# Kernel tuning notes

Hardware: AMD Instinct MI355X
Metric: run time of the kernel (lower is better)

Reference implementation:

```python
import jax, jax.numpy as jnp
import numpy as np

N_NODES = 100000
D = 128


def _sage_layer(h, src, dst, w_self, w_neigh, b):
    # GraphSAGE mean aggregation: mean of neighbor (src) features per dst node.
    msg = h[src]                                            # [E, D] gather
    agg = jax.ops.segment_sum(msg, dst, num_segments=N_NODES)  # [N, D]
    deg = jax.ops.segment_sum(jnp.ones(src.shape, h.dtype), dst, num_segments=N_NODES)
    mean = agg / jnp.maximum(deg, 1.0)[:, None]
    return h @ w_self + mean @ w_neigh + b


def setup_inputs() -> dict:
    key = jax.random.key(0)
    ks = jax.random.split(key, 16)
    E = 1600000
    inp = {
        "feat": jax.random.normal(ks[0], (N_NODES, D), jnp.float32),
        "edge0_src": jax.random.randint(ks[1], (E,), 0, N_NODES),
        "edge0_dst": jax.random.randint(ks[2], (E,), 0, N_NODES),
        "edge1_src": jax.random.randint(ks[3], (E,), 0, N_NODES),
        "edge1_dst": jax.random.randint(ks[4], (E,), 0, N_NODES),
        "pos_src": jax.random.randint(ks[5], (100000,), 0, N_NODES),
        "pos_dst": jax.random.randint(ks[6], (100000,), 0, N_NODES),
        "neg_src": jax.random.randint(ks[7], (500000,), 0, N_NODES),
        "neg_dst": jax.random.randint(ks[8], (500000,), 0, N_NODES),
        # learned parameters
        "w_proj": jax.random.normal(ks[9], (D, D), jnp.float32) / np.sqrt(D),
        "b_proj": jnp.zeros((D,), jnp.float32),
        "w_self1": jax.random.normal(ks[10], (D, D), jnp.float32) / np.sqrt(D),
        "w_neigh1": jax.random.normal(ks[11], (D, D), jnp.float32) / np.sqrt(D),
        "b1": jnp.zeros((D,), jnp.float32),
        "w_self2": jax.random.normal(ks[12], (D, D), jnp.float32) / np.sqrt(D),
        "w_neigh2": jax.random.normal(ks[13], (D, D), jnp.float32) / np.sqrt(D),
        "b2": jnp.zeros((D,), jnp.float32),
    }
    return inp


def reference(feat, edge0_src, edge0_dst, edge1_src, edge1_dst,
              pos_src, pos_dst, neg_src, neg_dst,
              w_proj, b_proj, w_self1, w_neigh1, b1, w_self2, w_neigh2, b2):
    # ProjectionLayer: per-node linear + ReLU on blocks[0].srcdata['feature']
    h = jax.nn.relu(feat @ w_proj + b_proj)
    # GNNLayer: one SAGE-mean layer per block
    h = jax.nn.relu(_sage_layer(h, edge0_src, edge0_dst, w_self1, w_neigh1, b1))
    h = _sage_layer(h, edge1_src, edge1_dst, w_self2, w_neigh2, b2)
    # PredictionLayer: dot-product edge scoring on pos_graph / neg_graph
    pos_score = jnp.sum(h[pos_src] * h[pos_dst], axis=-1)
    neg_score = jnp.sum(h[neg_src] * h[neg_dst], axis=-1)
    return (pos_score, neg_score)
```

## Files before the change

kernel.cpp:

```cpp
#include <hip/hip_runtime.h>
#include <hip/hip_bf16.h>

#define NN 100000
#define DD 128

#define NPB 512
#define NB 196
#define CAPB 12288
#define PA_BLOCKS 196

typedef unsigned short ushort_t;
typedef unsigned int uint_t;
typedef __attribute__((ext_vector_type(8))) short bf16x8;
typedef __attribute__((ext_vector_type(4))) float f32x4;

__device__ __forceinline__ ushort_t f2bf(float f) {
    uint_t u = __builtin_bit_cast(uint_t, f);
    u += 0x7FFFu + ((u >> 16) & 1u);
    return (ushort_t)(u >> 16);
}
__device__ __forceinline__ uint_t pack2bf(float a, float b) {
    return (uint_t)f2bf(a) | ((uint_t)f2bf(b) << 16);
}
__device__ __forceinline__ float bflo(uint_t v) {
    return __builtin_bit_cast(float, v << 16);
}
__device__ __forceinline__ float bfhi(uint_t v) {
    return __builtin_bit_cast(float, v & 0xFFFF0000u);
}

__device__ __forceinline__ void gload16(const ushort_t* g, ushort_t* l) {
    __builtin_amdgcn_global_load_lds(
        (const __attribute__((address_space(1))) void*)g,
        (__attribute__((address_space(3))) void*)l,
        16, 0, 0);
}

#define PREP_W_BLOCKS 320
#define PREP_Z_BLOCKS 3
__global__ __launch_bounds__(256) void prep(
    const float* __restrict__ w_proj,
    const float* __restrict__ w_self1, const float* __restrict__ w_neigh1,
    const float* __restrict__ w_self2, const float* __restrict__ w_neigh2,
    ushort_t* __restrict__ wtp, ushort_t* __restrict__ wt1,
    ushort_t* __restrict__ wt2, int* __restrict__ bcnt,
    ushort_t* __restrict__ h1pad, ushort_t* __restrict__ h2pad)
{
    const int bid = blockIdx.x;
    const int tid = threadIdx.x;
    if (bid < PREP_W_BLOCKS) {
        int which = bid >> 6;
        int t = (bid & 63) * 256 + tid;
        int n = t >> 7, k = t & 127;
        float v;
        ushort_t* d;
        switch (which) {
            case 0: v = w_proj  [(size_t)k * 128 + n]; d = wtp + (size_t)n * 128 + k;       break;
            case 1: v = w_self1 [(size_t)k * 128 + n]; d = wt1 + (size_t)n * 256 + k;       break;
            case 2: v = w_neigh1[(size_t)k * 128 + n]; d = wt1 + (size_t)n * 256 + 128 + k; break;
            case 3: v = w_self2 [(size_t)k * 128 + n]; d = wt2 + (size_t)n * 256 + k;       break;
            default:v = w_neigh2[(size_t)k * 128 + n]; d = wt2 + (size_t)n * 256 + 128 + k; break;
        }
        *d = f2bf(v);
    } else if (bid < PREP_W_BLOCKS + 2) {
        int i = (bid - PREP_W_BLOCKS) * 256 + tid;
        if (i < 2 * NB) bcnt[i] = 0;
    } else {
        uint_t* p1 = (uint_t*)h1pad;
        uint_t* p2 = (uint_t*)h2pad;
        if (tid < 64) p1[tid] = 0;
        else if (tid < 128) p2[tid - 64] = 0;
    }
}

template <bool RELU, bool TWO, bool CVT>
__global__ __launch_bounds__(256, 4) void gemm_bf16(
    const void* __restrict__ Av, const ushort_t* __restrict__ Bm,
    const ushort_t* __restrict__ W, const float* __restrict__ bias,
    ushort_t* __restrict__ outp)
{
    __shared__ char smem[32768];
    ushort_t* Ot = (ushort_t*)smem;

    const int tid  = threadIdx.x;
    const int lane = tid & 63;
    const int wav  = tid >> 6;
    const int row0 = blockIdx.x * 128;
    const int m0   = (wav & 1) * 64;
    const int n0   = (wav >> 1) * 64;
    const int KTOT = TWO ? 256 : 128;
    const int NCH  = TWO ? 8 : 4;

    f32x4 acc[4][4];
#pragma unroll
    for (int i = 0; i < 4; ++i)
#pragma unroll
        for (int j = 0; j < 4; ++j) acc[i][j] = (f32x4){0.f, 0.f, 0.f, 0.f};

    const int cl = lane & 15;
    const int q  = lane >> 4;

    if constexpr (CVT) {
        ushort_t* At = (ushort_t*)smem;
        ushort_t* Wt = (ushort_t*)(smem + 8192);
#pragma unroll 1
        for (int ch = 0; ch < NCH; ++ch) {
            const int kA = (ch & 3) * 32;
            const int kW = ch * 32;

            if (ch) __syncthreads();
#pragma unroll
            for (int j = 0; j < 2; ++j) {
                int cb = (j * 4 + wav) * 64;
                int c  = cb + lane;
                int r  = c >> 2, k2 = c & 3;
                gload16(W + (size_t)r * KTOT + kW + k2 * 8, Wt + cb * 8);
            }
            uint4 av[2];
            const float* fp = (const float*)Av;
#pragma unroll
            for (int j = 0; j < 2; ++j) {
                int g = tid + 256 * j;
                int r = g >> 2;
                int c = (g & 3) * 8;
                int grow = row0 + r;
                if (grow >= NN) grow = NN - 1;
                float4 f0 = *(const float4*)(fp + (size_t)grow * DD + kA + c);
                float4 f1 = *(const float4*)(fp + (size_t)grow * DD + kA + c + 4);
                av[j].x = pack2bf(f0.x, f0.y);
                av[j].y = pack2bf(f0.z, f0.w);
                av[j].z = pack2bf(f1.x, f1.y);
                av[j].w = pack2bf(f1.z, f1.w);
            }
#pragma unroll
            for (int j = 0; j < 2; ++j) {
                int g = tid + 256 * j;
                int r = g >> 2;
                int c = (g & 3) * 8;
                *(uint4*)(&At[r * 32 + c]) = av[j];
            }
            __syncthreads();

            bf16x8 af[4], bfr[4];
#pragma unroll
            for (int i = 0; i < 4; ++i)
                af[i] = *(const bf16x8*)(&At[(m0 + i * 16 + cl) * 32 + q * 8]);
#pragma unroll
            for (int j = 0; j < 4; ++j)
                bfr[j] = *(const bf16x8*)(&Wt[(n0 + j * 16 + cl) * 32 + q * 8]);
#pragma unroll
            for (int i = 0; i < 4; ++i)
#pragma unroll
                for (int j = 0; j < 4; ++j)
                    acc[i][j] = __builtin_amdgcn_mfma_f32_16x16x32_bf16(
                        af[i], bfr[j], acc[i][j], 0, 0, 0);
        }
    } else {
        auto STAGE = [&](int ch, int buf) {
            const bool second = TWO && (ch >= 4);
            const int kA = (ch & 3) * 32;
            const int kW = ch * 32;
            ushort_t* At = (ushort_t*)(smem + buf * 16384);
            ushort_t* Wt = At + 4096;
            const ushort_t* sp = second ? Bm : (const ushort_t*)Av;
#pragma unroll
            for (int j = 0; j < 2; ++j) {
                int cb = (j * 4 + wav) * 64;
                int c  = cb + lane;
                int r  = c >> 2, k2 = c & 3;
                int grow = row0 + r;
                if (grow >= NN) grow = NN - 1;
                gload16(sp + (size_t)grow * DD + kA + k2 * 8, At + cb * 8);
                gload16(W + (size_t)r * KTOT + kW + k2 * 8, Wt + cb * 8);
            }
        };
        auto COMPUTE = [&](int buf) {
            ushort_t* At = (ushort_t*)(smem + buf * 16384);
            ushort_t* Wt = At + 4096;
            bf16x8 af[4], bfr[4];
#pragma unroll
            for (int i = 0; i < 4; ++i)
                af[i] = *(const bf16x8*)(&At[(m0 + i * 16 + cl) * 32 + q * 8]);
#pragma unroll
            for (int j = 0; j < 4; ++j)
                bfr[j] = *(const bf16x8*)(&Wt[(n0 + j * 16 + cl) * 32 + q * 8]);
#pragma unroll
            for (int i = 0; i < 4; ++i)
#pragma unroll
                for (int j = 0; j < 4; ++j)
                    acc[i][j] = __builtin_amdgcn_mfma_f32_16x16x32_bf16(
                        af[i], bfr[j], acc[i][j], 0, 0, 0);
        };

        STAGE(0, 0);
        asm volatile("s_waitcnt vmcnt(0)" ::: "memory");
        __builtin_amdgcn_s_barrier();
        int cur = 0;
#pragma unroll 1
        for (int ch = 0; ch < NCH - 1; ++ch) {
            STAGE(ch + 1, cur ^ 1);
            COMPUTE(cur);
            asm volatile("s_waitcnt vmcnt(0)" ::: "memory");
            __builtin_amdgcn_s_barrier();
            cur ^= 1;
        }
        COMPUTE(cur);
    }

    __syncthreads();
#pragma unroll
    for (int j = 0; j < 4; ++j) {
        int c = n0 + j * 16 + cl;
        float bv = bias[c];
#pragma unroll
        for (int i = 0; i < 4; ++i) {
#pragma unroll
            for (int reg = 0; reg < 4; ++reg) {
                int r = m0 + i * 16 + 4 * q + reg;
                float v = acc[i][j][reg] + bv;
                if constexpr (RELU) v = fmaxf(v, 0.f);
                Ot[r * 128 + c] = f2bf(v);
            }
        }
    }
    __syncthreads();
    int rows = NN - row0; if (rows > 128) rows = 128;
    for (int t = tid; t < rows * 16; t += 256) {
        int r = t >> 4, c8 = (t & 15) * 8;
        *(uint4*)(outp + (size_t)(row0 + r) * DD + c8) =
            *(const uint4*)(&Ot[r * 128 + c8]);
    }
}

__global__ __launch_bounds__(256) void partA2(
    const int* __restrict__ e0s, const int* __restrict__ e0d, int E0,
    const int* __restrict__ e1s, const int* __restrict__ e1d, int E1,
    int* __restrict__ bcnt, uint_t* __restrict__ pairs)
{
    __shared__ int hist[NB];
    __shared__ int base[NB];
    const int tid  = threadIdx.x;
    const int half = blockIdx.x >= PA_BLOCKS;
    const int* __restrict__ src = half ? e1s : e0s;
    const int* __restrict__ dst = half ? e1d : e0d;
    const int E = half ? E1 : E0;
    int* bc = bcnt + half * NB;
    uint_t* pp = pairs + (size_t)half * NB * CAPB;
    const int blk = blockIdx.x - half * PA_BLOCKS;
    const int chunk = (E + PA_BLOCKS - 1) / PA_BLOCKS;
    const int ea = blk * chunk;
    int eb = ea + chunk; if (eb > E) eb = E;

    for (int b = tid; b < NB; b += 256) hist[b] = 0;
    __syncthreads();
    for (int e = ea + tid; e < eb; e += 256)
        atomicAdd(&hist[dst[e] >> 9], 1);
    __syncthreads();
    for (int b = tid; b < NB; b += 256) {
        base[b] = atomicAdd(&bc[b], hist[b]);
        hist[b] = 0;
    }
    __syncthreads();
    for (int e = ea + tid; e < eb; e += 256) {
        int d = dst[e];
        int b = d >> 9;
        int off = atomicAdd(&hist[b], 1);
        int p = base[b] + off;
        if (p < CAPB)
            pp[(size_t)b * CAPB + p] =
                ((uint_t)(d & (NPB - 1)) << 17) | (uint_t)src[e];
    }
}

__global__ __launch_bounds__(256, 2) void partB(
    uint_t* __restrict__ pairs, const int* __restrict__ bcnt,
    int* __restrict__ counts, int* __restrict__ offs)
{
    __shared__ int cnt[NPB];
    __shared__ int loff[NPB];
    __shared__ int ssc[256];
    __shared__ int image[CAPB];

    const int tid  = threadIdx.x;
    const int half = blockIdx.x >= NB;
    const int b    = blockIdx.x - half * NB;
    const int n0   = b << 9;
    int nb = NN - n0; if (nb > NPB) nb = NPB;
    int tot = bcnt[half * NB + b]; if (tot > CAPB) tot = CAPB;
    uint_t* pb = pairs + (size_t)(half * NB + b) * CAPB;
    const int gbase = (half * NB + b) * CAPB;
    int* cnts  = counts + (size_t)half * NN;
    int* offsl = offs   + (size_t)half * NN;

    for (int n = tid; n < NPB; n += 256) cnt[n] = 0;
    __syncthreads();
    for (int i = tid; i < tot; i += 256)
        atomicAdd(&cnt[pb[i] >> 17], 1);
    __syncthreads();

    int a0 = cnt[2 * tid], a1 = cnt[2 * tid + 1];
    int s = a0 + a1;
    ssc[tid] = s;
    __syncthreads();
    for (int off = 1; off < 256; off <<= 1) {
        int t = 0;
        if (tid >= off) t = ssc[tid - off];
        __syncthreads();
        if (tid >= off) ssc[tid] += t;
        __syncthreads();
    }
    int pre = ssc[tid] - s;
    loff[2 * tid]     = pre;
    loff[2 * tid + 1] = pre + a0;
    __syncthreads();

    for (int n = tid; n < nb; n += 256) {
        cnts[n0 + n]  = cnt[n];
        offsl[n0 + n] = gbase + loff[n];
    }
    for (int n = tid; n < NPB; n += 256) cnt[n] = 0;
    __syncthreads();

    for (int i = tid; i < tot; i += 256) {
        uint_t p = pb[i];
        int ln  = p >> 17;
        int pos = loff[ln] + atomicAdd(&cnt[ln], 1);
        image[pos] = (int)(p & 0x1FFFFu);
    }
    __syncthreads();
    for (int i = tid; i < tot; i += 256) pb[i] = (uint_t)image[i];
}

#define AGG_ISSUE(V, J)                                                   \
    do {                                                                  \
        int s_[8];                                                        \
        _Pragma("unroll")                                                 \
        for (int u = 0; u < 8; ++u) {                                     \
            int jj = (J) + u;                                             \
            int jc = jj < cnt ? jj : cnt - 1;                             \
            int sv = (int)csr[start + jc];                                \
            s_[u] = jj < cnt ? sv : NN;                                   \
        }                                                                 \
        _Pragma("unroll")                                                 \
        for (int u = 0; u < 8; ++u)                                       \
            V[u] = *(const uint4*)(hl + (size_t)s_[u] * DD);              \
    } while (0)

#define AGG_ACCUM(V)                                                      \
    do {                                                                  \
        _Pragma("unroll")                                                 \
        for (int u = 0; u < 8; ++u) {                                     \
            a0 += bflo(V[u].x); a1 += bfhi(V[u].x);                       \
            a2 += bflo(V[u].y); a3 += bfhi(V[u].y);                       \
            a4 += bflo(V[u].z); a5 += bfhi(V[u].z);                       \
            a6 += bflo(V[u].w); a7 += bfhi(V[u].w);                       \
        }                                                                 \
    } while (0)

__global__ __launch_bounds__(256) void aggregate_bf16(
    const ushort_t* __restrict__ h, const uint_t* __restrict__ csr,
    const int* __restrict__ offs, const int* __restrict__ counts,
    ushort_t* __restrict__ mean, int nn)
{
    int gid  = blockIdx.x * 256 + threadIdx.x;
    int node = gid >> 4;
    if (node >= nn) return;
    int lane  = gid & 15;
    int start = offs[node];
    int cnt   = counts[node];
    const ushort_t* __restrict__ hl = h + lane * 8;

    float a0 = 0.f, a1 = 0.f, a2 = 0.f, a3 = 0.f;
    float a4 = 0.f, a5 = 0.f, a6 = 0.f, a7 = 0.f;

    int nbt = (cnt + 7) >> 3;
    if (nbt > 0) {
        uint4 va[8], vb[8];
        AGG_ISSUE(va, 0);
        int j = 8, b = 1;
        for (; b + 1 < nbt; b += 2) {
            AGG_ISSUE(vb, j); j += 8;
            AGG_ACCUM(va);
            AGG_ISSUE(va, j); j += 8;
            AGG_ACCUM(vb);
        }
        if (b < nbt) {
            AGG_ISSUE(vb, j);
            AGG_ACCUM(va);
            AGG_ACCUM(vb);
        } else {
            AGG_ACCUM(va);
        }
    }

    float rinv = 1.0f / (float)(cnt > 1 ? cnt : 1);
    uint4 o;
    o.x = pack2bf(a0 * rinv, a1 * rinv);
    o.y = pack2bf(a2 * rinv, a3 * rinv);
    o.z = pack2bf(a4 * rinv, a5 * rinv);
    o.w = pack2bf(a6 * rinv, a7 * rinv);
    *(uint4*)(mean + (size_t)node * DD + lane * 8) = o;
}

__device__ __forceinline__ float dot8(uint4 a, uint4 b) {
    return bflo(a.x) * bflo(b.x) + bfhi(a.x) * bfhi(b.x)
         + bflo(a.y) * bflo(b.y) + bfhi(a.y) * bfhi(b.y)
         + bflo(a.z) * bflo(b.z) + bfhi(a.z) * bfhi(b.z)
         + bflo(a.w) * bflo(b.w) + bfhi(a.w) * bfhi(b.w);
}

__global__ __launch_bounds__(256) void score_both(
    const ushort_t* __restrict__ h,
    const int* __restrict__ ps, const int* __restrict__ pd,
    const int* __restrict__ ns, const int* __restrict__ nd,
    float* __restrict__ out, int EP, int TE)
{
    int gid = blockIdx.x * 256 + threadIdx.x;
    int grp = gid >> 4;
    int e0 = grp * 2;
    if (e0 >= TE) return;
    int lane = gid & 15;
    int e1 = e0 + 1;
    bool has1 = (e1 < TE);
    int ee = has1 ? e1 : e0;

    int s0, d0, s1, d1;
    if (e0 < EP) { s0 = ps[e0]; d0 = pd[e0]; }
    else         { s0 = ns[e0 - EP]; d0 = nd[e0 - EP]; }
    if (ee < EP) { s1 = ps[ee]; d1 = pd[ee]; }
    else         { s1 = ns[ee - EP]; d1 = nd[ee - EP]; }

    const ushort_t* __restrict__ hl = h + lane * 8;
    uint4 va0 = *(const uint4*)(hl + (size_t)s0 * DD);
    uint4 vb0 = *(const uint4*)(hl + (size_t)d0 * DD);
    uint4 va1 = *(const uint4*)(hl + (size_t)s1 * DD);
    uint4 vb1 = *(const uint4*)(hl + (size_t)d1 * DD);

    float r0 = dot8(va0, vb0);
    float r1 = dot8(va1, vb1);
#pragma unroll
    for (int off = 8; off; off >>= 1) {
        r0 += __shfl_down(r0, off, 16);
        r1 += __shfl_down(r1, off, 16);
    }
    if (lane == 0) {
        out[e0] = r0;
        if (has1) out[e1] = r1;
    }
}


extern "C" void kernel_launch(void* const* d_in, const int* in_sizes, int n_in,
                              void* d_out, int out_size, void* d_ws, size_t ws_size,
                              hipStream_t stream)
{
    const float* feat    = (const float*)d_in[0];
    const int*   e0s     = (const int*)d_in[1];
    const int*   e0d     = (const int*)d_in[2];
    const int*   e1s     = (const int*)d_in[3];
    const int*   e1d     = (const int*)d_in[4];
    const int*   ps      = (const int*)d_in[5];
    const int*   pd      = (const int*)d_in[6];
    const int*   ns      = (const int*)d_in[7];
    const int*   nd      = (const int*)d_in[8];
    const float* w_proj  = (const float*)d_in[9];
    const float* b_proj  = (const float*)d_in[10];
    const float* w_self1 = (const float*)d_in[11];
    const float* w_neigh1= (const float*)d_in[12];
    const float* b1      = (const float*)d_in[13];
    const float* w_self2 = (const float*)d_in[14];
    const float* w_neigh2= (const float*)d_in[15];
    const float* b2      = (const float*)d_in[16];

    float* out = (float*)d_out;

    const size_t NF  = (size_t)NN * DD;
    const size_t NFP = NF + DD;
    char* base = (char*)d_ws;

    ushort_t* h3   = (ushort_t*)base;
    ushort_t* h1   = h3 + NFP;
    ushort_t* mean = h1 + NFP;
    ushort_t* h2   = mean + NFP;

    uint_t* pairs  = (uint_t*)(h2 + NFP);
    int*    bcnt   = (int*)(pairs + (size_t)2 * NB * CAPB);
    int*    counts = bcnt + 2 * NB;
    int*    offs   = counts + 2 * NN;
    ushort_t* wts  = (ushort_t*)(offs + 2 * NN);
    ushort_t* wtp = wts;
    ushort_t* wt1 = wts + 128 * 128;
    ushort_t* wt2 = wt1 + 128 * 256;

    const int E0 = in_sizes[1];
    const int E1 = in_sizes[3];
    const int EP = in_sizes[5];
    const int EN = in_sizes[7];

    const int GB  = (NN + 127) / 128;
    const int AGB = (NN * 16 + 255) / 256;

    prep<<<PREP_W_BLOCKS + PREP_Z_BLOCKS, 256, 0, stream>>>(
        w_proj, w_self1, w_neigh1, w_self2, w_neigh2, wtp, wt1, wt2, bcnt,
        h1 + NF, h2 + NF);

    partA2<<<2 * PA_BLOCKS, 256, 0, stream>>>(
        e0s, e0d, E0, e1s, e1d, E1, bcnt, pairs);
    partB<<<2 * NB, 256, 0, stream>>>(pairs, bcnt, counts, offs);

    gemm_bf16<true, false, true><<<GB, 256, 0, stream>>>(
        feat, nullptr, wtp, b_proj, h1);

    aggregate_bf16<<<AGB, 256, 0, stream>>>(h1, pairs, offs, counts, mean, NN);
    gemm_bf16<true, true, false><<<GB, 256, 0, stream>>>(
        h1, mean, wt1, b1, h2);

    aggregate_bf16<<<AGB, 256, 0, stream>>>(
        h2, pairs, offs + NN, counts + NN, mean, NN);
    gemm_bf16<false, true, false><<<GB, 256, 0, stream>>>(
        h2, mean, wt2, b2, h3);

    const int TE = EP + EN;
    const int NG = (TE + 1) / 2;
    score_both<<<(NG * 16 + 255) / 256, 256, 0, stream>>>(
        h3, ps, pd, ns, nd, out, EP, TE);
}
```

Baseline: 398.8 us.

## Fuse projection GEMM and edge partition pass into one heterogeneous launch

```diff
diff --git a/kernel.cpp b/kernel.cpp
--- a/kernel.cpp
+++ b/kernel.cpp
@@ -8,6 +8,7 @@
 #define NB 196
 #define CAPB 12288
 #define PA_BLOCKS 196
+#define GBLK 782
 
 typedef unsigned short ushort_t;
 typedef unsigned int uint_t;
@@ -73,40 +74,39 @@
     }
 }
 
-template <bool RELU, bool TWO, bool CVT>
-__global__ __launch_bounds__(256, 4) void gemm_bf16(
-    const void* __restrict__ Av, const ushort_t* __restrict__ Bm,
-    const ushort_t* __restrict__ W, const float* __restrict__ bias,
-    ushort_t* __restrict__ outp)
+__global__ __launch_bounds__(256, 4) void gemm0_partA2(
+    const float* __restrict__ feat, const ushort_t* __restrict__ W,
+    const float* __restrict__ bias, ushort_t* __restrict__ outp,
+    const int* __restrict__ e0s, const int* __restrict__ e0d, int E0,
+    const int* __restrict__ e1s, const int* __restrict__ e1d, int E1,
+    int* __restrict__ bcnt, uint_t* __restrict__ pairs)
 {
     __shared__ char smem[32768];
-    ushort_t* Ot = (ushort_t*)smem;
-
-    const int tid  = threadIdx.x;
-    const int lane = tid & 63;
-    const int wav  = tid >> 6;
-    const int row0 = blockIdx.x * 128;
-    const int m0   = (wav & 1) * 64;
-    const int n0   = (wav >> 1) * 64;
-    const int KTOT = TWO ? 256 : 128;
-    const int NCH  = TWO ? 8 : 4;
-
-    f32x4 acc[4][4];
-#pragma unroll
-    for (int i = 0; i < 4; ++i)
-#pragma unroll
-        for (int j = 0; j < 4; ++j) acc[i][j] = (f32x4){0.f, 0.f, 0.f, 0.f};
-
-    const int cl = lane & 15;
-    const int q  = lane >> 4;
-
-    if constexpr (CVT) {
+    const int tid = threadIdx.x;
+
+    if (blockIdx.x < GBLK) {
         ushort_t* At = (ushort_t*)smem;
         ushort_t* Wt = (ushort_t*)(smem + 8192);
+        ushort_t* Ot = (ushort_t*)smem;
+
+        const int lane = tid & 63;
+        const int wav  = tid >> 6;
+        const int row0 = blockIdx.x * 128;
+        const int m0   = (wav & 1) * 64;
+        const int n0   = (wav >> 1) * 64;
+
+        f32x4 acc[4][4];
+#pragma unroll
+        for (int i = 0; i < 4; ++i)
+#pragma unroll
+            for (int j = 0; j < 4; ++j) acc[i][j] = (f32x4){0.f, 0.f, 0.f, 0.f};
+
+        const int cl = lane & 15;
+        const int q  = lane >> 4;
+
 #pragma unroll 1
-        for (int ch = 0; ch < NCH; ++ch) {
-            const int kA = (ch & 3) * 32;
-            const int kW = ch * 32;
+        for (int ch = 0; ch < 4; ++ch) {
+            const int kA = ch * 32;
 
             if (ch) __syncthreads();
 #pragma unroll
@@ -114,10 +114,9 @@
                 int cb = (j * 4 + wav) * 64;
                 int c  = cb + lane;
                 int r  = c >> 2, k2 = c & 3;
-                gload16(W + (size_t)r * KTOT + kW + k2 * 8, Wt + cb * 8);
+                gload16(W + (size_t)r * 128 + kA + k2 * 8, Wt + cb * 8);
             }
             uint4 av[2];
-            const float* fp = (const float*)Av;
 #pragma unroll
             for (int j = 0; j < 2; ++j) {
                 int g = tid + 256 * j;
@@ -125,8 +124,8 @@
                 int c = (g & 3) * 8;
                 int grow = row0 + r;
                 if (grow >= NN) grow = NN - 1;
-                float4 f0 = *(const float4*)(fp + (size_t)grow * DD + kA + c);
-                float4 f1 = *(const float4*)(fp + (size_t)grow * DD + kA + c + 4);
+                float4 f0 = *(const float4*)(feat + (size_t)grow * DD + kA + c);
+                float4 f1 = *(const float4*)(feat + (size_t)grow * DD + kA + c + 4);
                 av[j].x = pack2bf(f0.x, f0.y);
                 av[j].y = pack2bf(f0.z, f0.w);
                 av[j].z = pack2bf(f1.x, f1.y);
@@ -155,57 +154,144 @@
                     acc[i][j] = __builtin_amdgcn_mfma_f32_16x16x32_bf16(
                         af[i], bfr[j], acc[i][j], 0, 0, 0);
         }
+
+        __syncthreads();
+#pragma unroll
+        for (int j = 0; j < 4; ++j) {
+            int c = n0 + j * 16 + cl;
+            float bv = bias[c];
+#pragma unroll
+            for (int i = 0; i < 4; ++i) {
+#pragma unroll
+                for (int reg = 0; reg < 4; ++reg) {
+                    int r = m0 + i * 16 + 4 * q + reg;
+                    float v = acc[i][j][reg] + bv;
+                    v = fmaxf(v, 0.f);
+                    Ot[r * 128 + c] = f2bf(v);
+                }
+            }
+        }
+        __syncthreads();
+        int rows = NN - row0; if (rows > 128) rows = 128;
+        for (int t = tid; t < rows * 16; t += 256) {
+            int r = t >> 4, c8 = (t & 15) * 8;
+            *(uint4*)(outp + (size_t)(row0 + r) * DD + c8) =
+                *(const uint4*)(&Ot[r * 128 + c8]);
+        }
     } else {
-        auto STAGE = [&](int ch, int buf) {
-            const bool second = TWO && (ch >= 4);
-            const int kA = (ch & 3) * 32;
-            const int kW = ch * 32;
-            ushort_t* At = (ushort_t*)(smem + buf * 16384);
-            ushort_t* Wt = At + 4096;
-            const ushort_t* sp = second ? Bm : (const ushort_t*)Av;
-#pragma unroll
-            for (int j = 0; j < 2; ++j) {
-                int cb = (j * 4 + wav) * 64;
-                int c  = cb + lane;
-                int r  = c >> 2, k2 = c & 3;
-                int grow = row0 + r;
-                if (grow >= NN) grow = NN - 1;
-                gload16(sp + (size_t)grow * DD + kA + k2 * 8, At + cb * 8);
-                gload16(W + (size_t)r * KTOT + kW + k2 * 8, Wt + cb * 8);
-            }
-        };
-        auto COMPUTE = [&](int buf) {
-            ushort_t* At = (ushort_t*)(smem + buf * 16384);
-            ushort_t* Wt = At + 4096;
-            bf16x8 af[4], bfr[4];
-#pragma unroll
-            for (int i = 0; i < 4; ++i)
-                af[i] = *(const bf16x8*)(&At[(m0 + i * 16 + cl) * 32 + q * 8]);
+        int* hist = (int*)smem;
+        int* base = (int*)(smem + 1024);
+
+        const int bid  = blockIdx.x - GBLK;
+        const int half = bid >= PA_BLOCKS;
+        const int* __restrict__ src = half ? e1s : e0s;
+        const int* __restrict__ dst = half ? e1d : e0d;
+        const int E = half ? E1 : E0;
+        int* bc = bcnt + half * NB;
+        uint_t* pp = pairs + (size_t)half * NB * CAPB;
+        const int blk = bid - half * PA_BLOCKS;
+        const int chunk = (E + PA_BLOCKS - 1) / PA_BLOCKS;
+        const int ea = blk * chunk;
+        int eb = ea + chunk; if (eb > E) eb = E;
+
+        for (int b = tid; b < NB; b += 256) hist[b] = 0;
+        __syncthreads();
+        for (int e = ea + tid; e < eb; e += 256)
+            atomicAdd(&hist[dst[e] >> 9], 1);
+        __syncthreads();
+        for (int b = tid; b < NB; b += 256) {
+            base[b] = atomicAdd(&bc[b], hist[b]);
+            hist[b] = 0;
+        }
+        __syncthreads();
+        for (int e = ea + tid; e < eb; e += 256) {
+            int d = dst[e];
+            int b = d >> 9;
+            int off = atomicAdd(&hist[b], 1);
+            int p = base[b] + off;
+            if (p < CAPB)
+                pp[(size_t)b * CAPB + p] =
+                    ((uint_t)(d & (NPB - 1)) << 17) | (uint_t)src[e];
+        }
+    }
+}
+
+template <bool RELU>
+__global__ __launch_bounds__(256, 4) void gemm_bf16(
+    const ushort_t* __restrict__ Av, const ushort_t* __restrict__ Bm,
+    const ushort_t* __restrict__ W, const float* __restrict__ bias,
+    ushort_t* __restrict__ outp)
+{
+    __shared__ char smem[32768];
+    ushort_t* Ot = (ushort_t*)smem;
+
+    const int tid  = threadIdx.x;
+    const int lane = tid & 63;
+    const int wav  = tid >> 6;
+    const int row0 = blockIdx.x * 128;
+    const int m0   = (wav & 1) * 64;
+    const int n0   = (wav >> 1) * 64;
+    const int KTOT = 256;
+    const int NCH  = 8;
+
+    f32x4 acc[4][4];
+#pragma unroll
+    for (int i = 0; i < 4; ++i)
+#pragma unroll
+        for (int j = 0; j < 4; ++j) acc[i][j] = (f32x4){0.f, 0.f, 0.f, 0.f};
+
+    const int cl = lane & 15;
+    const int q  = lane >> 4;
+
+    auto STAGE = [&](int ch, int buf) {
+        const bool second = (ch >= 4);
+        const int kA = (ch & 3) * 32;
+        const int kW = ch * 32;
+        ushort_t* At = (ushort_t*)(smem + buf * 16384);
+        ushort_t* Wt = At + 4096;
+        const ushort_t* sp = second ? Bm : Av;
+#pragma unroll
+        for (int j = 0; j < 2; ++j) {
+            int cb = (j * 4 + wav) * 64;
+            int c  = cb + lane;
+            int r  = c >> 2, k2 = c & 3;
+            int grow = row0 + r;
+            if (grow >= NN) grow = NN - 1;
+            gload16(sp + (size_t)grow * DD + kA + k2 * 8, At + cb * 8);
+            gload16(W + (size_t)r * KTOT + kW + k2 * 8, Wt + cb * 8);
+        }
+    };
+    auto COMPUTE = [&](int buf) {
+        ushort_t* At = (ushort_t*)(smem + buf * 16384);
+        ushort_t* Wt = At + 4096;
+        bf16x8 af[4], bfr[4];
+#pragma unroll
+        for (int i = 0; i < 4; ++i)
+            af[i] = *(const bf16x8*)(&At[(m0 + i * 16 + cl) * 32 + q * 8]);
+#pragma unroll
+        for (int j = 0; j < 4; ++j)
+            bfr[j] = *(const bf16x8*)(&Wt[(n0 + j * 16 + cl) * 32 + q * 8]);
+#pragma unroll
+        for (int i = 0; i < 4; ++i)
 #pragma unroll
             for (int j = 0; j < 4; ++j)
-                bfr[j] = *(const bf16x8*)(&Wt[(n0 + j * 16 + cl) * 32 + q * 8]);
-#pragma unroll
-            for (int i = 0; i < 4; ++i)
-#pragma unroll
-                for (int j = 0; j < 4; ++j)
-                    acc[i][j] = __builtin_amdgcn_mfma_f32_16x16x32_bf16(
-                        af[i], bfr[j], acc[i][j], 0, 0, 0);
-        };
-
-        STAGE(0, 0);
+                acc[i][j] = __builtin_amdgcn_mfma_f32_16x16x32_bf16(
+                    af[i], bfr[j], acc[i][j], 0, 0, 0);
+    };
+
+    STAGE(0, 0);
+    asm volatile("s_waitcnt vmcnt(0)" ::: "memory");
+    __builtin_amdgcn_s_barrier();
+    int cur = 0;
+#pragma unroll 1
+    for (int ch = 0; ch < NCH - 1; ++ch) {
+        STAGE(ch + 1, cur ^ 1);
+        COMPUTE(cur);
         asm volatile("s_waitcnt vmcnt(0)" ::: "memory");
         __builtin_amdgcn_s_barrier();
-        int cur = 0;
-#pragma unroll 1
-        for (int ch = 0; ch < NCH - 1; ++ch) {
-            STAGE(ch + 1, cur ^ 1);
-            COMPUTE(cur);
-            asm volatile("s_waitcnt vmcnt(0)" ::: "memory");
-            __builtin_amdgcn_s_barrier();
-            cur ^= 1;
-        }
-        COMPUTE(cur);
-    }
+        cur ^= 1;
+    }
+    COMPUTE(cur);
 
     __syncthreads();
 #pragma unroll
@@ -229,46 +315,6 @@
         int r = t >> 4, c8 = (t & 15) * 8;
         *(uint4*)(outp + (size_t)(row0 + r) * DD + c8) =
             *(const uint4*)(&Ot[r * 128 + c8]);
-    }
-}
-
-__global__ __launch_bounds__(256) void partA2(
-    const int* __restrict__ e0s, const int* __restrict__ e0d, int E0,
-    const int* __restrict__ e1s, const int* __restrict__ e1d, int E1,
-    int* __restrict__ bcnt, uint_t* __restrict__ pairs)
-{
-    __shared__ int hist[NB];
-    __shared__ int base[NB];
-    const int tid  = threadIdx.x;
-    const int half = blockIdx.x >= PA_BLOCKS;
-    const int* __restrict__ src = half ? e1s : e0s;
-    const int* __restrict__ dst = half ? e1d : e0d;
-    const int E = half ? E1 : E0;
-    int* bc = bcnt + half * NB;
-    uint_t* pp = pairs + (size_t)half * NB * CAPB;
-    const int blk = blockIdx.x - half * PA_BLOCKS;
-    const int chunk = (E + PA_BLOCKS - 1) / PA_BLOCKS;
-    const int ea = blk * chunk;
-    int eb = ea + chunk; if (eb > E) eb = E;
-
-    for (int b = tid; b < NB; b += 256) hist[b] = 0;
-    __syncthreads();
-    for (int e = ea + tid; e < eb; e += 256)
-        atomicAdd(&hist[dst[e] >> 9], 1);
-    __syncthreads();
-    for (int b = tid; b < NB; b += 256) {
-        base[b] = atomicAdd(&bc[b], hist[b]);
-        hist[b] = 0;
-    }
-    __syncthreads();
-    for (int e = ea + tid; e < eb; e += 256) {
-        int d = dst[e];
-        int b = d >> 9;
-        int off = atomicAdd(&hist[b], 1);
-        int p = base[b] + off;
-        if (p < CAPB)
-            pp[(size_t)b * CAPB + p] =
-                ((uint_t)(d & (NPB - 1)) << 17) | (uint_t)src[e];
     }
 }
 
@@ -497,28 +543,23 @@
     const int EP = in_sizes[5];
     const int EN = in_sizes[7];
 
-    const int GB  = (NN + 127) / 128;
     const int AGB = (NN * 16 + 255) / 256;
 
     prep<<<PREP_W_BLOCKS + PREP_Z_BLOCKS, 256, 0, stream>>>(
         w_proj, w_self1, w_neigh1, w_self2, w_neigh2, wtp, wt1, wt2, bcnt,
         h1 + NF, h2 + NF);
 
-    partA2<<<2 * PA_BLOCKS, 256, 0, stream>>>(
-        e0s, e0d, E0, e1s, e1d, E1, bcnt, pairs);
+    gemm0_partA2<<<GBLK + 2 * PA_BLOCKS, 256, 0, stream>>>(
+        feat, wtp, b_proj, h1, e0s, e0d, E0, e1s, e1d, E1, bcnt, pairs);
+
     partB<<<2 * NB, 256, 0, stream>>>(pairs, bcnt, counts, offs);
 
-    gemm_bf16<true, false, true><<<GB, 256, 0, stream>>>(
-        feat, nullptr, wtp, b_proj, h1);
-
     aggregate_bf16<<<AGB, 256, 0, stream>>>(h1, pairs, offs, counts, mean, NN);
-    gemm_bf16<true, true, false><<<GB, 256, 0, stream>>>(
-        h1, mean, wt1, b1, h2);
+    gemm_bf16<true><<<GBLK, 256, 0, stream>>>(h1, mean, wt1, b1, h2);
 
     aggregate_bf16<<<AGB, 256, 0, stream>>>(
         h2, pairs, offs + NN, counts + NN, mean, NN);
-    gemm_bf16<false, true, false><<<GB, 256, 0, stream>>>(
-        h2, mean, wt2, b2, h3);
+    gemm_bf16<false><<<GBLK, 256, 0, stream>>>(h2, mean, wt2, b2, h3);
 
     const int TE = EP + EN;
     const int NG = (TE + 1) / 2;
```

After: 402.7 us. Within noise of the previous version (+1.0%).
